# Optimization experiments

Measured on AMD Instinct MI355X. Metric: run time of the kernel, lower is better.

## Reference

```python
import jax, jax.numpy as jnp
import numpy as np

N_NODES = 50000
N_EDGES = 800000
N_GRAPHS = 64
NEG_SLOPE = 0.2
LN_EPS = 1e-5


def setup_inputs() -> dict:
    key = jax.random.key(0)
    ks = jax.random.split(key, 20)
    s = 0.1
    inp = {
        "x": jax.random.normal(ks[0], (N_NODES, 8), jnp.float32),
        "edge_index": jax.random.randint(ks[1], (2, N_EDGES), 0, N_NODES, dtype=jnp.int32),
        "edge_attr": jax.random.uniform(ks[2], (N_EDGES, 1), jnp.float32),
        "batch": jnp.sort(jax.random.randint(ks[3], (N_NODES,), 0, N_GRAPHS, dtype=jnp.int32)),
        "Wl1": jax.random.normal(ks[4], (8, 256), jnp.float32) * s,
        "Wr1": jax.random.normal(ks[5], (8, 256), jnp.float32) * s,
        "We1": jax.random.normal(ks[6], (1, 256), jnp.float32) * s,
        "att1": jax.random.normal(ks[7], (4, 64), jnp.float32) * s,
        "b1": jnp.zeros((256,), jnp.float32),
        "g1": jnp.ones((256,), jnp.float32),
        "beta1": jnp.zeros((256,), jnp.float32),
        "Wl2": jax.random.normal(ks[8], (256, 128), jnp.float32) * s,
        "Wr2": jax.random.normal(ks[9], (256, 128), jnp.float32) * s,
        "We2": jax.random.normal(ks[10], (1, 128), jnp.float32) * s,
        "att2": jax.random.normal(ks[11], (1, 128), jnp.float32) * s,
        "b2": jnp.zeros((128,), jnp.float32),
        "g2": jnp.ones((128,), jnp.float32),
        "beta2": jnp.zeros((128,), jnp.float32),
    }
    return inp


def _gatv2(x, src, dst, ea, Wl, Wr, We, att, bias, heads, ch, concat):
    """PyG GATv2Conv with add_self_loops=True (fill_value='mean' for edge_attr)."""
    n = x.shape[0]
    # self-loop edge_attr = scatter-mean of edge_attr onto target node
    deg = jax.ops.segment_sum(jnp.ones((src.shape[0],), x.dtype), dst, num_segments=n)
    loop_attr = jax.ops.segment_sum(ea, dst, num_segments=n) / jnp.maximum(deg, 1.0)[:, None]
    loop_idx = jnp.arange(n, dtype=src.dtype)
    src2 = jnp.concatenate([src, loop_idx])
    dst2 = jnp.concatenate([dst, loop_idx])
    ea2 = jnp.concatenate([ea, loop_attr], axis=0)           # (E2, edge_dim)

    xl = (x @ Wl).reshape(n, heads, ch)   # source transform
    xr = (x @ Wr).reshape(n, heads, ch)   # target transform
    e = (ea2 @ We).reshape(-1, heads, ch)

    m = xl[src2] + xr[dst2] + e           # (E2, H, C)
    m = jnp.where(m > 0, m, NEG_SLOPE * m)  # LeakyReLU(0.2)
    alpha = jnp.einsum('ehc,hc->eh', m, att)  # (E2, H)
    # softmax over edges grouped by destination node
    amax = jax.ops.segment_max(alpha, dst2, num_segments=n)
    alpha = jnp.exp(alpha - amax[dst2])
    denom = jax.ops.segment_sum(alpha, dst2, num_segments=n)
    alpha = alpha / (denom[dst2] + 1e-16)

    out = jax.ops.segment_sum(alpha[:, :, None] * xl[src2], dst2, num_segments=n)  # (N,H,C)
    out = out.reshape(n, heads * ch) if concat else out.mean(axis=1)
    return out + bias


def _layernorm(x, g, b):
    mu = x.mean(-1, keepdims=True)
    var = ((x - mu) ** 2).mean(-1, keepdims=True)
    return (x - mu) * jax.lax.rsqrt(var + LN_EPS) * g + b


def reference(x, edge_index, edge_attr, batch,
              Wl1, Wr1, We1, att1, b1, g1, beta1,
              Wl2, Wr2, We2, att2, b2, g2, beta2):
    src, dst = edge_index[0], edge_index[1]
    h = _gatv2(x, src, dst, edge_attr, Wl1, Wr1, We1, att1, b1, 4, 64, True)
    h = jax.nn.elu(_layernorm(h, g1, beta1))
    h = _gatv2(h, src, dst, edge_attr, Wl2, Wr2, We2, att2, b2, 1, 128, False)
    h = jax.nn.elu(_layernorm(h, g2, beta2))
    cnt = jax.ops.segment_sum(jnp.ones((h.shape[0],), h.dtype), batch, num_segments=N_GRAPHS)
    pooled = jax.ops.segment_sum(h, batch, num_segments=N_GRAPHS) / jnp.maximum(cnt, 1.0)[:, None]
    return pooled  # (B, 128)
```

## Files before the change

kernel.cpp:

```cpp
#include <hip/hip_runtime.h>
#include <math.h>

#define N_NODES 50000
#define N_EDGES 800000
#define N_GRAPHS 64
#define NREP 32
#define LN_EPS 1e-5f
#define SCAN_BLKS 196

typedef __attribute__((ext_vector_type(8))) short bf16x8;
typedef __attribute__((ext_vector_type(4))) float f32x4;
typedef __attribute__((ext_vector_type(2))) _Float16 half2v;

template <int CTRL>
__device__ __forceinline__ float dppadd(float v) {
  int t = __builtin_amdgcn_update_dpp(0, __float_as_int(v), CTRL, 0xF, 0xF, true);
  return v + __int_as_float(t);
}
__device__ __forceinline__ float red16d(float p) {
  p = dppadd<0xB1>(p);
  p = dppadd<0x4E>(p);
  p = dppadd<0x141>(p);
  p = dppadd<0x140>(p);
  return p;
}
__device__ __forceinline__ float red64(float p) {
  p = red16d(p);
  p += __shfl_xor(p, 16); p += __shfl_xor(p, 32);
  return p;
}

__device__ __forceinline__ unsigned f2bf(float f) {
  unsigned u = __float_as_uint(f);
  return (u + 0x7fffu + ((u >> 16) & 1u)) >> 16;
}
__device__ __forceinline__ float bflo(unsigned u) { return __uint_as_float(u << 16); }
__device__ __forceinline__ float bfhi(unsigned u) { return __uint_as_float(u & 0xffff0000u); }

__device__ __forceinline__ half2v u2h(unsigned u) {
  return __builtin_bit_cast(half2v, u);
}
__device__ __forceinline__ float dot8h(uint4 xh, unsigned w0, unsigned w1,
                                       unsigned w2, unsigned w3) {
#if __has_builtin(__builtin_amdgcn_fdot2)
  float s = __builtin_amdgcn_fdot2(u2h(xh.x), u2h(w0), 0.f, false);
  s = __builtin_amdgcn_fdot2(u2h(xh.y), u2h(w1), s, false);
  s = __builtin_amdgcn_fdot2(u2h(xh.z), u2h(w2), s, false);
  s = __builtin_amdgcn_fdot2(u2h(xh.w), u2h(w3), s, false);
  return s;
#else
  float s = 0.f;
  half2v a;
  a = u2h(xh.x); { half2v b = u2h(w0); s += (float)a.x*(float)b.x + (float)a.y*(float)b.y; }
  a = u2h(xh.y); { half2v b = u2h(w1); s += (float)a.x*(float)b.x + (float)a.y*(float)b.y; }
  a = u2h(xh.z); { half2v b = u2h(w2); s += (float)a.x*(float)b.x + (float)a.y*(float)b.y; }
  a = u2h(xh.w); { half2v b = u2h(w3); s += (float)a.x*(float)b.x + (float)a.y*(float)b.y; }
  return s;
#endif
}

__global__ void k_hist(const int* __restrict__ dst, const float* __restrict__ ea,
                       int* __restrict__ deg, float* __restrict__ easum) {
  int e = blockIdx.x * 256 + threadIdx.x;
  if (e >= N_EDGES) return;
  int d = dst[e];
  atomicAdd(&deg[d], 1);
  atomicAdd(&easum[d], ea[e]);
}

__global__ void k_scanA(const int* __restrict__ deg, int* __restrict__ part) {
  int t = threadIdx.x;
  int i = blockIdx.x * 256 + t;
  int len = (i < N_NODES) ? ((deg[i] + 4) & ~3) : 0;
  __shared__ int sm[256];
  sm[t] = len; __syncthreads();
  for (int o = 128; o > 0; o >>= 1) {
    if (t < o) sm[t] += sm[t + o];
    __syncthreads();
  }
  if (t == 0) part[blockIdx.x] = sm[0];
}
__global__ void k_scanB(const int* __restrict__ part, int* __restrict__ base) {
  int t = threadIdx.x;
  __shared__ int sm[256];
  int v = (t < SCAN_BLKS) ? part[t] : 0;
  sm[t] = v; __syncthreads();
  for (int o = 1; o < 256; o <<= 1) {
    int u = (t >= o) ? sm[t - o] : 0;
    __syncthreads();
    sm[t] += u;
    __syncthreads();
  }
  base[t] = (t == 0) ? 0 : sm[t - 1];
}
__global__ void k_scanC(const int* __restrict__ deg, const int* __restrict__ base,
                        const float* __restrict__ easum,
                        int* __restrict__ off2,
                        int* __restrict__ ssrc, float* __restrict__ sea) {
  int t = threadIdx.x;
  int i = blockIdx.x * 256 + t;
  int d = (i < N_NODES) ? deg[i] : 0;
  int len = (i < N_NODES) ? ((d + 4) & ~3) : 0;
  __shared__ int sm[256];
  sm[t] = len; __syncthreads();
  for (int o = 1; o < 256; o <<= 1) {
    int u = (t >= o) ? sm[t - o] : 0;
    __syncthreads();
    sm[t] += u;
    __syncthreads();
  }
  int incl = sm[t];
  if (i < N_NODES) {
    int b = base[blockIdx.x] + incl - len;
    off2[i] = b;
    ssrc[b + d] = i;
    sea[b + d]  = easum[i] / fmaxf((float)d, 1.0f);
    for (int j = d + 1; j < len; ++j) { ssrc[b + j] = -1; sea[b + j] = 0.f; }
  }
  if (i == N_NODES - 1) off2[N_NODES] = base[blockIdx.x] + incl;
}

__global__ void k_scatter(const int* __restrict__ src, const int* __restrict__ dst,
                          const float* __restrict__ ea, const int* __restrict__ off2,
                          int* __restrict__ cursor, int* __restrict__ ssrc,
                          float* __restrict__ sea) {
  int e = blockIdx.x * 256 + threadIdx.x;
  if (e >= N_EDGES) return;
  int d = dst[e];
  int pos = off2[d] + atomicAdd(&cursor[d], 1);
  ssrc[pos] = src[e];
  sea[pos]  = ea[e];
}

__global__ void k_prep(const float* __restrict__ x, uint4* __restrict__ xh,
                       const float* __restrict__ Wl1, unsigned* __restrict__ Wlh,
                       const float* __restrict__ Wl2, const float* __restrict__ Wr2,
                       unsigned short* __restrict__ Btp) {
  int b = blockIdx.x, t = threadIdx.x;
  if (b < SCAN_BLKS) {
    int n = b * 256 + t;
    if (n >= N_NODES) return;
    float4 a = *(const float4*)(x + n * 8);
    float4 c = *(const float4*)(x + n * 8 + 4);
    half2v p0 = {(_Float16)a.x, (_Float16)a.y};
    half2v p1 = {(_Float16)a.z, (_Float16)a.w};
    half2v p2 = {(_Float16)c.x, (_Float16)c.y};
    half2v p3 = {(_Float16)c.z, (_Float16)c.w};
    xh[n] = make_uint4(__builtin_bit_cast(unsigned, p0), __builtin_bit_cast(unsigned, p1),
                       __builtin_bit_cast(unsigned, p2), __builtin_bit_cast(unsigned, p3));
  } else if (b < SCAN_BLKS + 4) {
    int kp = b - SCAN_BLKS;
    half2v h = {(_Float16)Wl1[(2 * kp) * 256 + t], (_Float16)Wl1[(2 * kp + 1) * 256 + t]};
    Wlh[kp * 256 + t] = __builtin_bit_cast(unsigned, h);
  } else {
    int nIdx = b - SCAN_BLKS - 4;
    float v = (nIdx < 128) ? Wl2[t * 128 + nIdx] : Wr2[t * 128 + (nIdx - 128)];
    Btp[nIdx * 256 + t] = (unsigned short)f2bf(v);
  }
}

__global__ __launch_bounds__(256) void k_gat1(
    const float* __restrict__ x, const uint4* __restrict__ xh16,
    const unsigned* __restrict__ Wlh,
    const float* __restrict__ Wr, const float* __restrict__ We,
    const float* __restrict__ att,
    const float* __restrict__ b1, const float* __restrict__ g1,
    const float* __restrict__ be1,
    const int* __restrict__ off2, const int* __restrict__ ssrc,
    const float* __restrict__ sea, unsigned* __restrict__ h1b) {
  int lane = threadIdx.x & 63;
  int wv = __builtin_amdgcn_readfirstlane(threadIdx.x >> 6);
  int n = blockIdx.x * 4 + wv;
  int c0 = lane * 4;

  float4 wev = *(const float4*)(We + c0);
  float4 atv = *(const float4*)(att + c0);

  float xn[8];
  {
    float4 a = *(const float4*)(x + n * 8);
    float4 b = *(const float4*)(x + n * 8 + 4);
    xn[0]=a.x; xn[1]=a.y; xn[2]=a.z; xn[3]=a.w;
    xn[4]=b.x; xn[5]=b.y; xn[6]=b.z; xn[7]=b.w;
  }
  float xr0=0.f, xr1=0.f, xr2=0.f, xr3=0.f;
#pragma unroll
  for (int k = 0; k < 8; ++k) {
    float4 wr = *(const float4*)(Wr + k * 256 + c0);
    xr0 += xn[k]*wr.x; xr1 += xn[k]*wr.y; xr2 += xn[k]*wr.z; xr3 += xn[k]*wr.w;
  }
  uint4 wk0 = *(const uint4*)(Wlh + 0 * 256 + c0);
  uint4 wk1 = *(const uint4*)(Wlh + 1 * 256 + c0);
  uint4 wk2 = *(const uint4*)(Wlh + 2 * 256 + c0);
  uint4 wk3 = *(const uint4*)(Wlh + 3 * 256 + c0);

  int beg   = __builtin_amdgcn_readfirstlane(off2[n]);
  int pairs = __builtin_amdgcn_readfirstlane((off2[n + 1] - beg) >> 1);

  float den = 0.f, ac0=0.f, ac1=0.f, ac2=0.f, ac3=0.f;

  int   sA = __builtin_amdgcn_readfirstlane(ssrc[beg]);
  int   sB = __builtin_amdgcn_readfirstlane(ssrc[beg + 1]);
  float eA = sea[beg], eB = sea[beg + 1];
  uint4 xA = xh16[max(sA, 0)];
  uint4 xB = xh16[max(sB, 0)];

  for (int p = 0; p < pairs; ++p) {
    int   csA = sA, csB = sB;
    float ceA = eA, ceB = eB;
    uint4 cxA = xA, cxB = xB;
    if (p + 1 < pairs) {
      int j = beg + 2 * (p + 1);
      sA = __builtin_amdgcn_readfirstlane(ssrc[j]);
      sB = __builtin_amdgcn_readfirstlane(ssrc[j + 1]);
      eA = sea[j];  eB = sea[j + 1];
      xA = xh16[max(sA, 0)];
      xB = xh16[max(sB, 0)];
    }
    float vA0 = dot8h(cxA, wk0.x, wk1.x, wk2.x, wk3.x);
    float vA1 = dot8h(cxA, wk0.y, wk1.y, wk2.y, wk3.y);
    float vA2 = dot8h(cxA, wk0.z, wk1.z, wk2.z, wk3.z);
    float vA3 = dot8h(cxA, wk0.w, wk1.w, wk2.w, wk3.w);
    float vB0 = dot8h(cxB, wk0.x, wk1.x, wk2.x, wk3.x);
    float vB1 = dot8h(cxB, wk0.y, wk1.y, wk2.y, wk3.y);
    float vB2 = dot8h(cxB, wk0.z, wk1.z, wk2.z, wk3.z);
    float vB3 = dot8h(cxB, wk0.w, wk1.w, wk2.w, wk3.w);

    float mA0 = vA0 + fmaf(ceA, wev.x, xr0); mA0 = fmaxf(mA0, 0.2f*mA0);
    float mA1 = vA1 + fmaf(ceA, wev.y, xr1); mA1 = fmaxf(mA1, 0.2f*mA1);
    float mA2 = vA2 + fmaf(ceA, wev.z, xr2); mA2 = fmaxf(mA2, 0.2f*mA2);
    float mA3 = vA3 + fmaf(ceA, wev.w, xr3); mA3 = fmaxf(mA3, 0.2f*mA3);
    float mB0 = vB0 + fmaf(ceB, wev.x, xr0); mB0 = fmaxf(mB0, 0.2f*mB0);
    float mB1 = vB1 + fmaf(ceB, wev.y, xr1); mB1 = fmaxf(mB1, 0.2f*mB1);
    float mB2 = vB2 + fmaf(ceB, wev.z, xr2); mB2 = fmaxf(mB2, 0.2f*mB2);
    float mB3 = vB3 + fmaf(ceB, wev.w, xr3); mB3 = fmaxf(mB3, 0.2f*mB3);

    float pA = mA0*atv.x + mA1*atv.y + mA2*atv.z + mA3*atv.w;
    float pB = mB0*atv.x + mB1*atv.y + mB2*atv.z + mB3*atv.w;
    pA = red16d(pA);
    pB = red16d(pB);

    float wA = (csA >= 0) ? __expf(pA) : 0.f;
    float wB = (csB >= 0) ? __expf(pB) : 0.f;
    den += wA + wB;
    ac0 = fmaf(wA, vA0, fmaf(wB, vB0, ac0));
    ac1 = fmaf(wA, vA1, fmaf(wB, vB1, ac1));
    ac2 = fmaf(wA, vA2, fmaf(wB, vB2, ac2));
    ac3 = fmaf(wA, vA3, fmaf(wB, vB3, ac3));
  }

  float inv = 1.0f / (den + 1e-16f);
  float4 bv = *(const float4*)(b1 + c0);
  float o0 = ac0*inv + bv.x, o1 = ac1*inv + bv.y;
  float o2 = ac2*inv + bv.z, o3 = ac3*inv + bv.w;
  float mu = red64(o0 + o1 + o2 + o3) * (1.0f / 256.0f);
  float d0 = o0-mu, d1 = o1-mu, d2 = o2-mu, d3 = o3-mu;
  float rstd = rsqrtf(red64(d0*d0 + d1*d1 + d2*d2 + d3*d3) * (1.0f/256.0f) + LN_EPS);
  float4 gv  = *(const float4*)(g1 + c0);
  float4 bev = *(const float4*)(be1 + c0);
  float y0 = d0*rstd*gv.x + bev.x; y0 = y0 > 0.f ? y0 : __expf(y0) - 1.0f;
  float y1 = d1*rstd*gv.y + bev.y; y1 = y1 > 0.f ? y1 : __expf(y1) - 1.0f;
  float y2 = d2*rstd*gv.z + bev.z; y2 = y2 > 0.f ? y2 : __expf(y2) - 1.0f;
  float y3 = d3*rstd*gv.w + bev.w; y3 = y3 > 0.f ? y3 : __expf(y3) - 1.0f;
  unsigned lo = f2bf(y0) | (f2bf(y1) << 16);
  unsigned hi = f2bf(y2) | (f2bf(y3) << 16);
  *(uint2*)(h1b + (size_t)n * 128 + lane * 2) = make_uint2(lo, hi);
}

__global__ __launch_bounds__(256) void k_gemm2(
    const unsigned* __restrict__ h1b, const unsigned short* __restrict__ Btp,
    unsigned short* __restrict__ xl2b, float* __restrict__ xr2) {
  __shared__ unsigned short Ash[64][264];
  __shared__ unsigned short Bsh[64][264];
  int t = threadIdx.x;
  int bm0 = blockIdx.x * 64;
  int n0  = blockIdx.y * 64;

#pragma unroll
  for (int i = 0; i < 8; ++i) {
    int idx = t + 256 * i;
    int row = idx >> 5, c4 = idx & 31;
    int gm = bm0 + row;
    uint4 va = (gm < N_NODES) ? *(const uint4*)(h1b + (size_t)gm * 128 + c4 * 4)
                              : make_uint4(0,0,0,0);
    *(uint4*)(&Ash[row][c4 * 8]) = va;
    uint4 vb = *(const uint4*)((const unsigned*)Btp + (size_t)(n0 + row) * 128 + c4 * 4);
    *(uint4*)(&Bsh[row][c4 * 8]) = vb;
  }
  __syncthreads();

  int lane = t & 63, w = t >> 6;
  int lm = lane & 15, lk = (lane >> 4) * 8;
  f32x4 acc[4];
#pragma unroll
  for (int i = 0; i < 4; ++i) acc[i] = (f32x4){0.f,0.f,0.f,0.f};

#pragma unroll
  for (int kk = 0; kk < 8; ++kk) {
    bf16x8 a = *(const bf16x8*)(&Ash[16*w + lm][kk*32 + lk]);
#pragma unroll
    for (int tt = 0; tt < 4; ++tt) {
      bf16x8 b = *(const bf16x8*)(&Bsh[16*tt + lm][kk*32 + lk]);
      acc[tt] = __builtin_amdgcn_mfma_f32_16x16x32_bf16(a, b, acc[tt], 0, 0, 0);
    }
  }

#pragma unroll
  for (int tt = 0; tt < 4; ++tt) {
#pragma unroll
    for (int r = 0; r < 4; ++r) {
      int node = bm0 + 16*w + (lane >> 4) * 4 + r;
      if (node < N_NODES) {
        int colg = n0 + tt * 16 + lm;
        float v = acc[tt][r];
        if (colg < 128) xl2b[(size_t)node * 128 + colg] = (unsigned short)f2bf(v);
        else            xr2 [(size_t)node * 128 + (colg - 128)] = v;
      }
    }
  }
}

__global__ __launch_bounds__(256) void k_gat2(
    const unsigned* __restrict__ xl2b, const float* __restrict__ xr2,
    const float* __restrict__ We, const float* __restrict__ att,
    const float* __restrict__ b2, const float* __restrict__ g2,
    const float* __restrict__ be2,
    const int* __restrict__ off2, const int* __restrict__ ssrc,
    const float* __restrict__ sea,
    const int* __restrict__ batch,
    float* __restrict__ pool, float* __restrict__ cnt) {
  int tid = threadIdx.x;
  int lane = tid & 63;
  int wv = __builtin_amdgcn_readfirstlane(tid >> 6);
  int row = lane >> 4, col = lane & 15;
  int n = blockIdx.x * 4 + wv;
  int c0 = col * 8;
  int cu0 = col * 4;

  float wev[8], at[8], xr[8];
  *(float4*)(wev)     = *(const float4*)(We + c0);
  *(float4*)(wev + 4) = *(const float4*)(We + c0 + 4);
  *(float4*)(at)      = *(const float4*)(att + c0);
  *(float4*)(at + 4)  = *(const float4*)(att + c0 + 4);
  *(float4*)(xr)      = *(const float4*)(xr2 + (size_t)n * 128 + c0);
  *(float4*)(xr + 4)  = *(const float4*)(xr2 + (size_t)n * 128 + c0 + 4);

  int beg   = __builtin_amdgcn_readfirstlane(off2[n]);
  int quads = __builtin_amdgcn_readfirstlane((off2[n + 1] - beg) >> 2);

  float den = 0.f;
  float ac[8] = {0,0,0,0,0,0,0,0};

  int s0 = -1, s1 = -1, s2 = -1;
  float e0 = 0.f, e1 = 0.f, e2 = 0.f;
  uint4 u0 = make_uint4(0,0,0,0), u1 = u0, u2 = u0;
  {
    s0 = ssrc[beg + row]; e0 = sea[beg + row];
    u0 = *(const uint4*)(xl2b + (size_t)max(s0, 0) * 64 + cu0);
  }
  if (quads > 1) {
    s1 = ssrc[beg + 4 + row]; e1 = sea[beg + 4 + row];
    u1 = *(const uint4*)(xl2b + (size_t)max(s1, 0) * 64 + cu0);
  }
  if (quads > 2) {
    s2 = ssrc[beg + 8 + row]; e2 = sea[beg + 8 + row];
    u2 = *(const uint4*)(xl2b + (size_t)max(s2, 0) * 64 + cu0);
  }

  for (int q = 0; q < quads; ++q) {
    int cs = s0; float ce = e0; uint4 cu = u0;
    s0 = s1; e0 = e1; u0 = u1;
    s1 = s2; e1 = e2; u1 = u2;
    if (q + 3 < quads) {
      int j = beg + (q + 3) * 4 + row;
      s2 = ssrc[j]; e2 = sea[j];
      u2 = *(const uint4*)(xl2b + (size_t)max(s2, 0) * 64 + cu0);
    }
    float v[8];
    v[0]=bflo(cu.x); v[1]=bfhi(cu.x); v[2]=bflo(cu.y); v[3]=bfhi(cu.y);
    v[4]=bflo(cu.z); v[5]=bfhi(cu.z); v[6]=bflo(cu.w); v[7]=bfhi(cu.w);
    float p = 0.f;
#pragma unroll
    for (int j = 0; j < 8; ++j) {
      float m = v[j] + fmaf(ce, wev[j], xr[j]);
      m = fmaxf(m, 0.2f * m);
      p = fmaf(m, at[j], p);
    }
    p = red16d(p);
    float w = (cs >= 0) ? __expf(p) : 0.f;
    den += w;
#pragma unroll
    for (int j = 0; j < 8; ++j) ac[j] = fmaf(w, v[j], ac[j]);
  }
  den += __shfl_xor(den, 16); den += __shfl_xor(den, 32);
#pragma unroll
  for (int j = 0; j < 8; ++j) {
    ac[j] += __shfl_xor(ac[j], 16);
    ac[j] += __shfl_xor(ac[j], 32);
  }

  float inv = 1.0f / (den + 1e-16f);
  float o[8], y[8];
  float bv[8], gv[8], bev[8];
  *(float4*)(bv)      = *(const float4*)(b2 + c0);
  *(float4*)(bv + 4)  = *(const float4*)(b2 + c0 + 4);
  *(float4*)(gv)      = *(const float4*)(g2 + c0);
  *(float4*)(gv + 4)  = *(const float4*)(g2 + c0 + 4);
  *(float4*)(bev)     = *(const float4*)(be2 + c0);
  *(float4*)(bev + 4) = *(const float4*)(be2 + c0 + 4);
  float osum = 0.f;
#pragma unroll
  for (int j = 0; j < 8; ++j) { o[j] = ac[j] * inv + bv[j]; osum += o[j]; }
  float mu = red64(osum) * (1.0f / 512.0f);
  float vsum = 0.f;
#pragma unroll
  for (int j = 0; j < 8; ++j) { o[j] -= mu; vsum += o[j] * o[j]; }
  float rstd = rsqrtf(red64(vsum) * (1.0f / 512.0f) + LN_EPS);
#pragma unroll
  for (int j = 0; j < 8; ++j) {
    float t2 = o[j] * rstd * gv[j] + bev[j];
    y[j] = t2 > 0.f ? t2 : __expf(t2) - 1.0f;
  }

  __shared__ float pbuf[4][128];
  __shared__ int gbuf[4];
  if (row == 0) {
#pragma unroll
    for (int j = 0; j < 8; ++j) pbuf[wv][c0 + j] = y[j];
  }
  if (lane == 0) gbuf[wv] = batch[n];
  __syncthreads();
  if (wv == 0) {
    int r = blockIdx.x & (NREP - 1);
    int ch = lane;
    float acc0 = pbuf[0][ch], acc1 = pbuf[0][ch+64];
    int cg = gbuf[0], cn = 1;
#pragma unroll
    for (int i = 1; i < 4; ++i) {
      if (gbuf[i] == cg) { acc0 += pbuf[i][ch]; acc1 += pbuf[i][ch+64]; cn++; }
      else {
        float* pp = pool + ((size_t)(r * N_GRAPHS + cg)) * 128;
        atomicAdd(pp + ch, acc0); atomicAdd(pp + ch + 64, acc1);
        if (lane == 0) atomicAdd(&cnt[r * N_GRAPHS + cg], (float)cn);
        cg = gbuf[i]; acc0 = pbuf[i][ch]; acc1 = pbuf[i][ch+64]; cn = 1;
      }
    }
    float* pp = pool + ((size_t)(r * N_GRAPHS + cg)) * 128;
    atomicAdd(pp + ch, acc0); atomicAdd(pp + ch + 64, acc1);
    if (lane == 0) atomicAdd(&cnt[r * N_GRAPHS + cg], (float)cn);
  }
}

__global__ void k_final(const float* __restrict__ pool, const float* __restrict__ cnt,
                        float* __restrict__ out) {
  int idx = blockIdx.x * 256 + threadIdx.x;
  if (idx >= N_GRAPHS * 128) return;
  int g = idx >> 7, c = idx & 127;
  float s = 0.f, nn = 0.f;
#pragma unroll
  for (int r = 0; r < NREP; ++r) {
    s  += pool[((size_t)(r * N_GRAPHS + g)) * 128 + c];
    nn += cnt[r * N_GRAPHS + g];
  }
  out[idx] = s / fmaxf(nn, 1.0f);
}

extern "C" void kernel_launch(void* const* d_in, const int* in_sizes, int n_in,
                              void* d_out, int out_size, void* d_ws, size_t ws_size,
                              hipStream_t stream) {
  const float* x    = (const float*)d_in[0];
  const int*   ei   = (const int*)  d_in[1];
  const float* ea   = (const float*)d_in[2];
  const int*   batch= (const int*)  d_in[3];
  const float* Wl1  = (const float*)d_in[4];
  const float* Wr1  = (const float*)d_in[5];
  const float* We1  = (const float*)d_in[6];
  const float* att1 = (const float*)d_in[7];
  const float* b1   = (const float*)d_in[8];
  const float* g1   = (const float*)d_in[9];
  const float* be1  = (const float*)d_in[10];
  const float* Wl2  = (const float*)d_in[11];
  const float* Wr2  = (const float*)d_in[12];
  const float* We2  = (const float*)d_in[13];
  const float* att2 = (const float*)d_in[14];
  const float* b2   = (const float*)d_in[15];
  const float* g2   = (const float*)d_in[16];
  const float* be2  = (const float*)d_in[17];
  const int* srcp = ei;
  const int* dstp = ei + N_EDGES;

  const int MAXE2 = N_EDGES + 4 * N_NODES;

  char* ws = (char*)d_ws;
  size_t off = 0;
  auto alloc = [&](size_t bytes) {
    char* p = ws + off; off += (bytes + 15) & ~(size_t)15; return p;
  };
  int*            deg   = (int*)           alloc((size_t)N_NODES * 4);
  float*          easum = (float*)         alloc((size_t)N_NODES * 4);
  int*            cursor= (int*)           alloc((size_t)N_NODES * 4);
  int*            off2  = (int*)           alloc((size_t)(N_NODES + 1) * 4);
  int*            part  = (int*)           alloc((size_t)256 * 4);
  int*            base  = (int*)           alloc((size_t)257 * 4);
  int*            ssrc  = (int*)           alloc((size_t)MAXE2 * 4);
  float*          sea   = (float*)         alloc((size_t)MAXE2 * 4);
  uint4*          xh16  = (uint4*)         alloc((size_t)N_NODES * 16);
  unsigned*       Wlh   = (unsigned*)      alloc((size_t)4 * 256 * 4);
  unsigned*       h1b   = (unsigned*)      alloc((size_t)N_NODES * 128 * 4);
  unsigned short* xl2b  = (unsigned short*)alloc((size_t)N_NODES * 128 * 2);
  float*          xr2   = (float*)         alloc((size_t)N_NODES * 128 * 4);
  unsigned short* Btp   = (unsigned short*)alloc((size_t)256 * 256 * 2);
  float*          pool  = (float*)         alloc((size_t)NREP * N_GRAPHS * 128 * 4);
  float*          cnt   = (float*)         alloc((size_t)NREP * N_GRAPHS * 4);

  (void)hipMemsetAsync(deg, 0, (char*)off2 - (char*)deg, stream);
  (void)hipMemsetAsync(pool, 0, ((char*)cnt + (((size_t)NREP*N_GRAPHS*4 + 15) & ~(size_t)15))
                           - (char*)pool, stream);

  k_hist    <<<N_EDGES / 256, 256, 0, stream>>>(dstp, ea, deg, easum);
  k_prep    <<<SCAN_BLKS + 4 + 256, 256, 0, stream>>>(x, xh16, Wl1, Wlh, Wl2, Wr2, Btp);
  k_scanA   <<<SCAN_BLKS, 256, 0, stream>>>(deg, part);
  k_scanB   <<<1, 256, 0, stream>>>(part, base);
  k_scanC   <<<SCAN_BLKS, 256, 0, stream>>>(deg, base, easum, off2, ssrc, sea);
  k_scatter <<<N_EDGES / 256, 256, 0, stream>>>(srcp, dstp, ea, off2, cursor, ssrc, sea);
  k_gat1    <<<N_NODES / 4, 256, 0, stream>>>(x, xh16, Wlh, Wr1, We1, att1, b1, g1, be1,
                                              off2, ssrc, sea, h1b);
  dim3 g7((N_NODES + 63) / 64, 4);
  k_gemm2   <<<g7, 256, 0, stream>>>(h1b, Btp, xl2b, xr2);
  k_gat2    <<<N_NODES / 4, 256, 0, stream>>>((const unsigned*)xl2b, xr2, We2, att2,
                                              b2, g2, be2,
                                              off2, ssrc, sea, batch, pool, cnt);
  k_final   <<<(N_GRAPHS * 128) / 256, 256, 0, stream>>>(pool, cnt, (float*)d_out);
}
```

Measured before the change: 437.2 us.

## Interleave CSR src/edge-attr into uint2 records and reuse A tile across GEMM panels

```diff
diff --git a/kernel.cpp b/kernel.cpp
--- a/kernel.cpp
+++ b/kernel.cpp
@@ -95,8 +95,7 @@
 }
 __global__ void k_scanC(const int* __restrict__ deg, const int* __restrict__ base,
                         const float* __restrict__ easum,
-                        int* __restrict__ off2,
-                        int* __restrict__ ssrc, float* __restrict__ sea) {
+                        int* __restrict__ off2, uint2* __restrict__ sent) {
   int t = threadIdx.x;
   int i = blockIdx.x * 256 + t;
   int d = (i < N_NODES) ? deg[i] : 0;
@@ -113,23 +112,21 @@
   if (i < N_NODES) {
     int b = base[blockIdx.x] + incl - len;
     off2[i] = b;
-    ssrc[b + d] = i;
-    sea[b + d]  = easum[i] / fmaxf((float)d, 1.0f);
-    for (int j = d + 1; j < len; ++j) { ssrc[b + j] = -1; sea[b + j] = 0.f; }
+    float lea = easum[i] / fmaxf((float)d, 1.0f);
+    sent[b + d] = make_uint2((unsigned)i, __float_as_uint(lea));
+    for (int j = d + 1; j < len; ++j) sent[b + j] = make_uint2(0xFFFFFFFFu, 0u);
   }
   if (i == N_NODES - 1) off2[N_NODES] = base[blockIdx.x] + incl;
 }
 
 __global__ void k_scatter(const int* __restrict__ src, const int* __restrict__ dst,
                           const float* __restrict__ ea, const int* __restrict__ off2,
-                          int* __restrict__ cursor, int* __restrict__ ssrc,
-                          float* __restrict__ sea) {
+                          int* __restrict__ cursor, uint2* __restrict__ sent) {
   int e = blockIdx.x * 256 + threadIdx.x;
   if (e >= N_EDGES) return;
   int d = dst[e];
   int pos = off2[d] + atomicAdd(&cursor[d], 1);
-  ssrc[pos] = src[e];
-  sea[pos]  = ea[e];
+  sent[pos] = make_uint2((unsigned)src[e], __float_as_uint(ea[e]));
 }
 
 __global__ void k_prep(const float* __restrict__ x, uint4* __restrict__ xh,
@@ -166,8 +163,8 @@
     const float* __restrict__ att,
     const float* __restrict__ b1, const float* __restrict__ g1,
     const float* __restrict__ be1,
-    const int* __restrict__ off2, const int* __restrict__ ssrc,
-    const float* __restrict__ sea, unsigned* __restrict__ h1b) {
+    const int* __restrict__ off2, const uint2* __restrict__ sent,
+    unsigned* __restrict__ h1b) {
   int lane = threadIdx.x & 63;
   int wv = __builtin_amdgcn_readfirstlane(threadIdx.x >> 6);
   int n = blockIdx.x * 4 + wv;
@@ -199,9 +196,10 @@
 
   float den = 0.f, ac0=0.f, ac1=0.f, ac2=0.f, ac3=0.f;
 
-  int   sA = __builtin_amdgcn_readfirstlane(ssrc[beg]);
-  int   sB = __builtin_amdgcn_readfirstlane(ssrc[beg + 1]);
-  float eA = sea[beg], eB = sea[beg + 1];
+  uint4 pr = *(const uint4*)(sent + beg);
+  int   sA = __builtin_amdgcn_readfirstlane((int)pr.x);
+  int   sB = __builtin_amdgcn_readfirstlane((int)pr.z);
+  float eA = __uint_as_float(pr.y), eB = __uint_as_float(pr.w);
   uint4 xA = xh16[max(sA, 0)];
   uint4 xB = xh16[max(sB, 0)];
 
@@ -210,10 +208,10 @@
     float ceA = eA, ceB = eB;
     uint4 cxA = xA, cxB = xB;
     if (p + 1 < pairs) {
-      int j = beg + 2 * (p + 1);
-      sA = __builtin_amdgcn_readfirstlane(ssrc[j]);
-      sB = __builtin_amdgcn_readfirstlane(ssrc[j + 1]);
-      eA = sea[j];  eB = sea[j + 1];
+      pr = *(const uint4*)(sent + beg + 2 * (p + 1));
+      sA = __builtin_amdgcn_readfirstlane((int)pr.x);
+      sB = __builtin_amdgcn_readfirstlane((int)pr.z);
+      eA = __uint_as_float(pr.y); eB = __uint_as_float(pr.w);
       xA = xh16[max(sA, 0)];
       xB = xh16[max(sB, 0)];
     }
@@ -274,7 +272,8 @@
   __shared__ unsigned short Bsh[64][264];
   int t = threadIdx.x;
   int bm0 = blockIdx.x * 64;
-  int n0  = blockIdx.y * 64;
+  int lane = t & 63, w = t >> 6;
+  int lm = lane & 15, lk = (lane >> 4) * 8;
 
 #pragma unroll
   for (int i = 0; i < 8; ++i) {
@@ -284,39 +283,46 @@
     uint4 va = (gm < N_NODES) ? *(const uint4*)(h1b + (size_t)gm * 128 + c4 * 4)
                               : make_uint4(0,0,0,0);
     *(uint4*)(&Ash[row][c4 * 8]) = va;
-    uint4 vb = *(const uint4*)((const unsigned*)Btp + (size_t)(n0 + row) * 128 + c4 * 4);
-    *(uint4*)(&Bsh[row][c4 * 8]) = vb;
-  }
-  __syncthreads();
-
-  int lane = t & 63, w = t >> 6;
-  int lm = lane & 15, lk = (lane >> 4) * 8;
-  f32x4 acc[4];
-#pragma unroll
-  for (int i = 0; i < 4; ++i) acc[i] = (f32x4){0.f,0.f,0.f,0.f};
-
-#pragma unroll
-  for (int kk = 0; kk < 8; ++kk) {
-    bf16x8 a = *(const bf16x8*)(&Ash[16*w + lm][kk*32 + lk]);
+  }
+
+  for (int pnl = 0; pnl < 4; ++pnl) {
+    int n0 = pnl * 64;
+#pragma unroll
+    for (int i = 0; i < 8; ++i) {
+      int idx = t + 256 * i;
+      int row = idx >> 5, c4 = idx & 31;
+      uint4 vb = *(const uint4*)((const unsigned*)Btp + (size_t)(n0 + row) * 128 + c4 * 4);
+      *(uint4*)(&Bsh[row][c4 * 8]) = vb;
+    }
+    __syncthreads();
+
+    f32x4 acc[4];
+#pragma unroll
+    for (int i = 0; i < 4; ++i) acc[i] = (f32x4){0.f,0.f,0.f,0.f};
+#pragma unroll
+    for (int kk = 0; kk < 8; ++kk) {
+      bf16x8 a = *(const bf16x8*)(&Ash[16*w + lm][kk*32 + lk]);
+#pragma unroll
+      for (int tt = 0; tt < 4; ++tt) {
+        bf16x8 b = *(const bf16x8*)(&Bsh[16*tt + lm][kk*32 + lk]);
+        acc[tt] = __builtin_amdgcn_mfma_f32_16x16x32_bf16(a, b, acc[tt], 0, 0, 0);
+      }
+    }
+
 #pragma unroll
     for (int tt = 0; tt < 4; ++tt) {
-      bf16x8 b = *(const bf16x8*)(&Bsh[16*tt + lm][kk*32 + lk]);
-      acc[tt] = __builtin_amdgcn_mfma_f32_16x16x32_bf16(a, b, acc[tt], 0, 0, 0);
-    }
-  }
-
-#pragma unroll
-  for (int tt = 0; tt < 4; ++tt) {
-#pragma unroll
-    for (int r = 0; r < 4; ++r) {
-      int node = bm0 + 16*w + (lane >> 4) * 4 + r;
-      if (node < N_NODES) {
-        int colg = n0 + tt * 16 + lm;
-        float v = acc[tt][r];
-        if (colg < 128) xl2b[(size_t)node * 128 + colg] = (unsigned short)f2bf(v);
-        else            xr2 [(size_t)node * 128 + (colg - 128)] = v;
+#pragma unroll
+      for (int r = 0; r < 4; ++r) {
+        int node = bm0 + 16*w + (lane >> 4) * 4 + r;
+        if (node < N_NODES) {
+          int colg = n0 + tt * 16 + lm;
+          float v = acc[tt][r];
+          if (colg < 128) xl2b[(size_t)node * 128 + colg] = (unsigned short)f2bf(v);
+          else            xr2 [(size_t)node * 128 + (colg - 128)] = v;
+        }
       }
     }
+    __syncthreads();
   }
 }
 
@@ -325,8 +331,7 @@
     const float* __restrict__ We, const float* __restrict__ att,
     const float* __restrict__ b2, const float* __restrict__ g2,
     const float* __restrict__ be2,
-    const int* __restrict__ off2, const int* __restrict__ ssrc,
-    const float* __restrict__ sea,
+    const int* __restrict__ off2, const uint2* __restrict__ sent,
     const int* __restrict__ batch,
     float* __restrict__ pool, float* __restrict__ cnt) {
   int tid = threadIdx.x;
@@ -355,15 +360,18 @@
   float e0 = 0.f, e1 = 0.f, e2 = 0.f;
   uint4 u0 = make_uint4(0,0,0,0), u1 = u0, u2 = u0;
   {
-    s0 = ssrc[beg + row]; e0 = sea[beg + row];
+    uint2 tt = sent[beg + row];
+    s0 = (int)tt.x; e0 = __uint_as_float(tt.y);
     u0 = *(const uint4*)(xl2b + (size_t)max(s0, 0) * 64 + cu0);
   }
   if (quads > 1) {
-    s1 = ssrc[beg + 4 + row]; e1 = sea[beg + 4 + row];
+    uint2 tt = sent[beg + 4 + row];
+    s1 = (int)tt.x; e1 = __uint_as_float(tt.y);
     u1 = *(const uint4*)(xl2b + (size_t)max(s1, 0) * 64 + cu0);
   }
   if (quads > 2) {
-    s2 = ssrc[beg + 8 + row]; e2 = sea[beg + 8 + row];
+    uint2 tt = sent[beg + 8 + row];
+    s2 = (int)tt.x; e2 = __uint_as_float(tt.y);
     u2 = *(const uint4*)(xl2b + (size_t)max(s2, 0) * 64 + cu0);
   }
 
@@ -372,8 +380,8 @@
     s0 = s1; e0 = e1; u0 = u1;
     s1 = s2; e1 = e2; u1 = u2;
     if (q + 3 < quads) {
-      int j = beg + (q + 3) * 4 + row;
-      s2 = ssrc[j]; e2 = sea[j];
+      uint2 tt = sent[beg + (q + 3) * 4 + row];
+      s2 = (int)tt.x; e2 = __uint_as_float(tt.y);
       u2 = *(const uint4*)(xl2b + (size_t)max(s2, 0) * 64 + cu0);
     }
     float v[8];
@@ -502,8 +510,7 @@
   int*            off2  = (int*)           alloc((size_t)(N_NODES + 1) * 4);
   int*            part  = (int*)           alloc((size_t)256 * 4);
   int*            base  = (int*)           alloc((size_t)257 * 4);
-  int*            ssrc  = (int*)           alloc((size_t)MAXE2 * 4);
-  float*          sea   = (float*)         alloc((size_t)MAXE2 * 4);
+  uint2*          sent  = (uint2*)         alloc((size_t)MAXE2 * 8);
   uint4*          xh16  = (uint4*)         alloc((size_t)N_NODES * 16);
   unsigned*       Wlh   = (unsigned*)      alloc((size_t)4 * 256 * 4);
   unsigned*       h1b   = (unsigned*)      alloc((size_t)N_NODES * 128 * 4);
@@ -521,14 +528,13 @@
   k_prep    <<<SCAN_BLKS + 4 + 256, 256, 0, stream>>>(x, xh16, Wl1, Wlh, Wl2, Wr2, Btp);
   k_scanA   <<<SCAN_BLKS, 256, 0, stream>>>(deg, part);
   k_scanB   <<<1, 256, 0, stream>>>(part, base);
-  k_scanC   <<<SCAN_BLKS, 256, 0, stream>>>(deg, base, easum, off2, ssrc, sea);
-  k_scatter <<<N_EDGES / 256, 256, 0, stream>>>(srcp, dstp, ea, off2, cursor, ssrc, sea);
+  k_scanC   <<<SCAN_BLKS, 256, 0, stream>>>(deg, base, easum, off2, sent);
+  k_scatter <<<N_EDGES / 256, 256, 0, stream>>>(srcp, dstp, ea, off2, cursor, sent);
   k_gat1    <<<N_NODES / 4, 256, 0, stream>>>(x, xh16, Wlh, Wr1, We1, att1, b1, g1, be1,
-                                              off2, ssrc, sea, h1b);
-  dim3 g7((N_NODES + 63) / 64, 4);
-  k_gemm2   <<<g7, 256, 0, stream>>>(h1b, Btp, xl2b, xr2);
+                                              off2, sent, h1b);
+  k_gemm2   <<<(N_NODES + 63) / 64, 256, 0, stream>>>(h1b, Btp, xl2b, xr2);
   k_gat2    <<<N_NODES / 4, 256, 0, stream>>>((const unsigned*)xl2b, xr2, We2, att2,
                                               b2, g2, be2,
-                                              off2, ssrc, sea, batch, pool, cnt);
+                                              off2, sent, batch, pool, cnt);
   k_final   <<<(N_GRAPHS * 128) / 256, 256, 0, stream>>>(pool, cnt, (float*)d_out);
 }
```

Result: faster. 415.3 us (-5.0%).
